# Optimization experiments

Hardware: AMD Instinct MI355X
Metric: run time of the kernel (lower is better)

## Reference

```python
import math
import jax, jax.numpy as jnp
import numpy as np

B, T, C = 4, 2048, 1024
H = 16
D = C // H  # head dim = 64


def setup_inputs() -> dict:
    key = jax.random.key(0)
    ks = jax.random.split(key, 9)
    s = 0.02
    return {
        "x": jax.random.normal(ks[0], (B, T, C), dtype=jnp.float32),
        "Wq": jax.random.normal(ks[1], (C, C), dtype=jnp.float32) * s,
        "bq": jax.random.normal(ks[2], (C,), dtype=jnp.float32) * s,
        "Wk": jax.random.normal(ks[3], (C, C), dtype=jnp.float32) * s,
        "bk": jax.random.normal(ks[4], (C,), dtype=jnp.float32) * s,
        "Wv": jax.random.normal(ks[5], (C, C), dtype=jnp.float32) * s,
        "bv": jax.random.normal(ks[6], (C,), dtype=jnp.float32) * s,
        "Wo": jax.random.normal(ks[7], (C, C), dtype=jnp.float32) * s,
        "bo": jax.random.normal(ks[8], (C,), dtype=jnp.float32) * s,
    }


def reference(x, Wq, bq, Wk, bk, Wv, bv, Wo, bo):
    # Linear projections (torch Linear: x @ W.T + b), split into heads -> [B,H,T,D]
    def heads(y):
        return y.reshape(B, T, H, D).transpose(0, 2, 1, 3)

    q = heads(x @ Wq.T + bq)
    k = heads(x @ Wk.T + bk)
    v = heads(x @ Wv.T + bv)

    # Full [B,H,T,T] score matrix, scaled by 1/sqrt(D) (no mask, dropout=0 / eval)
    scores = jnp.einsum("bhqd,bhkd->bhqk", q, k) / math.sqrt(D)
    attn = jax.nn.softmax(scores, axis=-1)
    out = jnp.einsum("bhqk,bhkd->bhqd", attn, v)
    out = out.transpose(0, 2, 1, 3).reshape(B, T, C)
    return out @ Wo.T + bo
```

## Files before the change

kernel.cpp:

```cpp
#include <hip/hip_runtime.h>
#include <hip/hip_bf16.h>
#include <stdint.h>

#define Bb 4
#define Tt 2048
#define Cc 1024
#define Hh 16
#define Dd 64

using bf16x8 = __bf16 __attribute__((ext_vector_type(8)));
using f32x4  = float  __attribute__((ext_vector_type(4)));
using f32x16 = float  __attribute__((ext_vector_type(16)));
typedef unsigned short u16;
typedef unsigned int   u32;

#if defined(__has_builtin) && __has_builtin(__builtin_amdgcn_exp2f)
#define EXP2F(x) __builtin_amdgcn_exp2f(x)
#else
#define EXP2F(x) exp2f(x)
#endif

#if defined(__has_builtin) && __has_builtin(__builtin_amdgcn_permlane32_swap)
#define PERMLANE32_SWAP(a, b)                                          \
  do {                                                                 \
    auto _r = __builtin_amdgcn_permlane32_swap((a), (b), false, false);\
    (a) = _r[0]; (b) = _r[1];                                          \
  } while (0)
#else
#define PERMLANE32_SWAP(a, b) \
  asm volatile("v_permlane32_swap_b32 %0, %1" : "+v"(a), "+v"(b))
#endif

__device__ __forceinline__ u16 f32_to_bf16(float f) {
  union { float f; unsigned u; } v; v.f = f;
  unsigned r = v.u + 0x7fffu + ((v.u >> 16) & 1u);
  return (u16)(r >> 16);
}

__device__ __forceinline__ void gl2lds16(const u16* g, u16* l) {
  __builtin_amdgcn_global_load_lds(
      (const __attribute__((address_space(1))) u32*)g,
      (__attribute__((address_space(3))) u32*)l, 16, 0, 0);
}

__global__ void cast_f32_to_bf16(const float* __restrict__ in, u16* __restrict__ out, int n) {
  int i = (blockIdx.x * blockDim.x + threadIdx.x) * 4;
  if (i >= n) return;
  float4 v = *reinterpret_cast<const float4*>(in + i);
  ushort4 o;
  o.x = f32_to_bf16(v.x); o.y = f32_to_bf16(v.y);
  o.z = f32_to_bf16(v.z); o.w = f32_to_bf16(v.w);
  *reinterpret_cast<ushort4*>(out + i) = o;
}

__global__ void cast4_f32_to_bf16(const float* __restrict__ w0, const float* __restrict__ w1,
                                  const float* __restrict__ w2, const float* __restrict__ w3,
                                  u16* __restrict__ o0, u16* __restrict__ o1,
                                  u16* __restrict__ o2, u16* __restrict__ o3, int n) {
  const float* in; u16* out;
  switch (blockIdx.y) {
    case 0: in = w0; out = o0; break;
    case 1: in = w1; out = o1; break;
    case 2: in = w2; out = o2; break;
    default: in = w3; out = o3; break;
  }
  int i = (blockIdx.x * blockDim.x + threadIdx.x) * 4;
  if (i >= n) return;
  float4 v = *reinterpret_cast<const float4*>(in + i);
  ushort4 o;
  o.x = f32_to_bf16(v.x); o.y = f32_to_bf16(v.y);
  o.z = f32_to_bf16(v.z); o.w = f32_to_bf16(v.w);
  *reinterpret_cast<ushort4*>(out + i) = o;
}

__global__ __launch_bounds__(256, 2)
void gemm_qkv(const u16* __restrict__ A, const u16* __restrict__ Bqkv,
              const float* __restrict__ bq, const float* __restrict__ bk,
              const float* __restrict__ bv,
              u16* __restrict__ qout, u16* __restrict__ kout, u16* __restrict__ vtout,
              float qscl)
{
  constexpr int K = Cc, BK = 32, LDT = 136;
  __shared__ alignas(16) u16 smem[128 * LDT];
  u16* As = smem;
  u16* Bs = smem + 128 * BK;
  const int tid  = threadIdx.x;
  const int wave = tid >> 6, lane = tid & 63;
  const int row0 = blockIdx.x * 128, col0 = blockIdx.y * 128;
  const int seg  = col0 >> 10;
  const int wm = (wave & 1) * 64, wn = (wave >> 1) * 64;
  const int fr = lane & 15, fk = (lane >> 4) * 8;
  const int srow = lane >> 2, scol = (lane & 3) * 8;

  f32x4 acc[4][4] = {};

  for (int k0 = 0; k0 < K; k0 += BK) {
#pragma unroll
    for (int c = 0; c < 2; ++c) {
      int rg = (wave * 2 + c) * 16;
      gl2lds16(A    + (size_t)(row0 + rg + srow) * K + k0 + scol, &As[rg * BK]);
      gl2lds16(Bqkv + (size_t)(col0 + rg + srow) * K + k0 + scol, &Bs[rg * BK]);
    }
    __syncthreads();
    bf16x8 af[4], bf[4];
#pragma unroll
    for (int i = 0; i < 4; ++i) {
      af[i] = *reinterpret_cast<const bf16x8*>(&As[(wm + i * 16 + fr) * BK + fk]);
      bf[i] = *reinterpret_cast<const bf16x8*>(&Bs[(wn + i * 16 + fr) * BK + fk]);
    }
#pragma unroll
    for (int i = 0; i < 4; ++i)
#pragma unroll
      for (int j = 0; j < 4; ++j)
        acc[i][j] = __builtin_amdgcn_mfma_f32_16x16x32_bf16(af[i], bf[j], acc[i][j], 0, 0, 0);
    __syncthreads();
  }

  const float* bias = (seg == 0) ? bq : ((seg == 1) ? bk : bv);
  const float scale = (seg == 0) ? qscl : 1.0f;
  const int colL0 = col0 & 1023;

  if (seg < 2) {
    u16* outp = (seg == 0) ? qout : kout;
#pragma unroll
    for (int j = 0; j < 4; ++j) {
      int col = colL0 + wn + j * 16 + fr;
      float bvv = bias[col];
#pragma unroll
      for (int i = 0; i < 4; ++i) {
        int rowb = row0 + wm + i * 16 + (lane >> 4) * 4;
#pragma unroll
        for (int r = 0; r < 4; ++r)
          outp[(size_t)(rowb + r) * Cc + col] = f32_to_bf16((acc[i][j][r] + bvv) * scale);
      }
    }
  } else {
#pragma unroll
    for (int j = 0; j < 4; ++j) {
      int lc = wn + j * 16 + fr;
      float bvv = bias[colL0 + lc];
#pragma unroll
      for (int i = 0; i < 4; ++i) {
        int lr = wm + i * 16 + (lane >> 4) * 4;
#pragma unroll
        for (int r = 0; r < 4; ++r)
          smem[lc * LDT + lr + r] = f32_to_bf16(acc[i][j][r] + bvv);
      }
    }
    __syncthreads();
    int lc = tid >> 1, seg2 = tid & 1;
    int col = colL0 + lc;
    int h = col >> 6, d = col & 63;
    int bb = row0 >> 11, t0 = (row0 & 2047) + seg2 * 64;
    u16* dst = vtout + ((size_t)(bb * Hh + h) * Dd + d) * Tt + t0;
    const u16* src = &smem[lc * LDT + seg2 * 64];
#pragma unroll
    for (int g = 0; g < 8; ++g)
      *reinterpret_cast<uint4*>(dst + g * 8) = *reinterpret_cast<const uint4*>(src + g * 8);
  }
}

__global__ __launch_bounds__(256, 2)
void gemm_out(const u16* __restrict__ A, const u16* __restrict__ Bw,
              const float* __restrict__ bias, float* __restrict__ Cout,
              int M, int N, int K)
{
  constexpr int BK = 32;
  __shared__ alignas(16) u16 As[128 * BK];
  __shared__ alignas(16) u16 Bs[128 * BK];
  const int tid  = threadIdx.x;
  const int wave = tid >> 6, lane = tid & 63;
  const int row0 = blockIdx.x * 128, col0 = blockIdx.y * 128;
  const int wm = (wave & 1) * 64, wn = (wave >> 1) * 64;
  const int fr = lane & 15, fk = (lane >> 4) * 8;
  const int srow = lane >> 2, scol = (lane & 3) * 8;

  f32x4 acc[4][4] = {};

  for (int k0 = 0; k0 < K; k0 += BK) {
#pragma unroll
    for (int c = 0; c < 2; ++c) {
      int rg = (wave * 2 + c) * 16;
      gl2lds16(A  + (size_t)(row0 + rg + srow) * K + k0 + scol, &As[rg * BK]);
      gl2lds16(Bw + (size_t)(col0 + rg + srow) * K + k0 + scol, &Bs[rg * BK]);
    }
    __syncthreads();
    bf16x8 af[4], bf[4];
#pragma unroll
    for (int i = 0; i < 4; ++i) {
      af[i] = *reinterpret_cast<const bf16x8*>(&As[(wm + i * 16 + fr) * BK + fk]);
      bf[i] = *reinterpret_cast<const bf16x8*>(&Bs[(wn + i * 16 + fr) * BK + fk]);
    }
#pragma unroll
    for (int i = 0; i < 4; ++i)
#pragma unroll
      for (int j = 0; j < 4; ++j)
        acc[i][j] = __builtin_amdgcn_mfma_f32_16x16x32_bf16(af[i], bf[j], acc[i][j], 0, 0, 0);
    __syncthreads();
  }

#pragma unroll
  for (int j = 0; j < 4; ++j) {
    int col = col0 + wn + j * 16 + fr;
    float bv = bias[col];
#pragma unroll
    for (int i = 0; i < 4; ++i) {
      int rowb = row0 + wm + i * 16 + (lane >> 4) * 4;
#pragma unroll
      for (int r = 0; r < 4; ++r)
        Cout[(size_t)(rowb + r) * N + col] = acc[i][j][r] + bv;
    }
  }
}

__global__ __launch_bounds__(256, 2)
void attn_kernel(const u16* __restrict__ Q, const u16* __restrict__ Kmat,
                 const u16* __restrict__ VT, u16* __restrict__ O) {
  __shared__ alignas(16) unsigned char smem[65536];
  float* OfT = (float*)smem;
  float* Qs  = (float*)(smem + 17408);

  const int tid = threadIdx.x, wave = tid >> 6, lane = tid & 63;
  const int l31 = lane & 31, hi = lane >> 5;
  const int bh = blockIdx.x, qt0 = blockIdx.y;
  const int b = bh >> 4, h = bh & 15;
  const size_t base = (size_t)b * Tt * Cc + (size_t)h * Dd;
  const size_t vtb = (size_t)bh * Dd * Tt;

  bf16x8 qb[2][4];
#pragma unroll
  for (int qt = 0; qt < 2; ++qt) {
    const u16* qp = Q + base + (size_t)(qt0 * 64 + qt * 32 + l31) * Cc + hi * 8;
#pragma unroll
    for (int c = 0; c < 4; ++c)
      qb[qt][c] = *reinterpret_cast<const bf16x8*>(qp + c * 16);
  }

  f32x16 Oacc[2][2] = {};
  float ssum[2] = {0.f, 0.f};

  const u16* pK = Kmat + base + (size_t)(wave * 32 + (lane >> 3)) * Cc +
                  (((lane & 7) ^ (lane >> 3)) << 3);
  const u16* pV[4];
#pragma unroll
  for (int c = 0; c < 4; ++c) {
    int d = wave * 16 + c * 4 + (lane >> 4);
    int cs = (lane & 15) ^ ((c << 2) + (lane >> 4));
    pV[c] = VT + vtb + (size_t)d * Tt + (cs << 3);
  }

  auto STAGE = [&](int buf, int kt) {
    u16* Kd = (u16*)(smem + (buf << 15)) + wave * 2048;
    u16* Vd = Kd + 8192;
    const u16* pk = pK + (size_t)kt * Cc;
#pragma unroll
    for (int c = 0; c < 4; ++c) {
      gl2lds16(pk + (size_t)(c * 8) * Cc, Kd + c * 512);
      gl2lds16(pV[c] + kt, Vd + c * 512);
    }
  };

  STAGE(0, 0);
  __syncthreads();

  int cur = 0;
#pragma unroll 1
  for (int t = 0; t < 16; ++t) {
    if (t < 15) STAGE(cur ^ 1, (t + 1) << 7);

    const u16* Ks = (const u16*)(smem + (cur << 15));
    const u16* Vs = Ks + 8192;

    bf16x8 ka[4], vb[2][2];
    const int key = wave * 32 + l31;
#pragma unroll
    for (int c = 0; c < 4; ++c)
      ka[c] = *reinterpret_cast<const bf16x8*>(
          &Ks[key * 64 + ((((c << 1) + hi) ^ (key & 7)) << 3)]);
#pragma unroll
    for (int k0i = 0; k0i < 2; ++k0i)
#pragma unroll
      for (int dh = 0; dh < 2; ++dh) {
        int drow = dh * 32 + l31;
        int ch = wave * 4 + k0i * 2 + hi;
        vb[k0i][dh] = *reinterpret_cast<const bf16x8*>(
            &Vs[drow * 128 + ((ch ^ (drow & 15)) << 3)]);
      }

#pragma unroll
    for (int qt = 0; qt < 2; ++qt) {
      f32x16 s = {};
#pragma unroll
      for (int c = 0; c < 4; ++c)
        s = __builtin_amdgcn_mfma_f32_32x32x16_bf16(ka[c], qb[qt][c], s, 0, 0, 0);
      unsigned pk8[8];
      float sm = 0.f;
#pragma unroll
      for (int i = 0; i < 8; ++i) {
        float p0 = EXP2F(s[2 * i]), p1 = EXP2F(s[2 * i + 1]);
        sm += p0 + p1;
        union { __hip_bfloat162 h2; unsigned u; } cv;
        cv.h2 = __float22bfloat162_rn(make_float2(p0, p1));
        pk8[i] = cv.u;
      }
      ssum[qt] += sm;
      unsigned a0 = pk8[0], a1 = pk8[1], a2 = pk8[2], a3 = pk8[3];
      unsigned b0 = pk8[4], b1 = pk8[5], b2 = pk8[6], b3 = pk8[7];
      PERMLANE32_SWAP(a0, a2);
      PERMLANE32_SWAP(a1, a3);
      PERMLANE32_SWAP(b0, b2);
      PERMLANE32_SWAP(b1, b3);
      union { unsigned u[4]; bf16x8 v; } plo, phi;
      plo.u[0] = a0; plo.u[1] = a1; plo.u[2] = a2; plo.u[3] = a3;
      phi.u[0] = b0; phi.u[1] = b1; phi.u[2] = b2; phi.u[3] = b3;
      Oacc[qt][0] = __builtin_amdgcn_mfma_f32_32x32x16_bf16(plo.v, vb[0][0], Oacc[qt][0], 0, 0, 0);
      Oacc[qt][1] = __builtin_amdgcn_mfma_f32_32x32x16_bf16(plo.v, vb[0][1], Oacc[qt][1], 0, 0, 0);
      Oacc[qt][0] = __builtin_amdgcn_mfma_f32_32x32x16_bf16(phi.v, vb[1][0], Oacc[qt][0], 0, 0, 0);
      Oacc[qt][1] = __builtin_amdgcn_mfma_f32_32x32x16_bf16(phi.v, vb[1][1], Oacc[qt][1], 0, 0, 0);
    }
    __syncthreads();
    cur ^= 1;
  }

#pragma unroll
  for (int qt = 0; qt < 2; ++qt) {
    float s = ssum[qt];
    s += __shfl_xor(s, 32, 64);
    if (hi == 0) Qs[wave * 64 + qt * 32 + l31] = s;
  }

  for (int w = 0; w < 4; ++w) {
    if (wave == w) {
#pragma unroll
      for (int qt = 0; qt < 2; ++qt)
#pragma unroll
        for (int dh = 0; dh < 2; ++dh) {
          int d = dh * 32 + l31;
          float* rowp = &OfT[d * 68 + qt * 32 + hi * 4];
#pragma unroll
          for (int g = 0; g < 4; ++g) {
            f32x4 v;
            v[0] = Oacc[qt][dh][g * 4 + 0]; v[1] = Oacc[qt][dh][g * 4 + 1];
            v[2] = Oacc[qt][dh][g * 4 + 2]; v[3] = Oacc[qt][dh][g * 4 + 3];
            float* dst = rowp + g * 8;
            if (w == 0) *reinterpret_cast<f32x4*>(dst) = v;
            else {
              f32x4 old = *reinterpret_cast<const f32x4*>(dst);
              *reinterpret_cast<f32x4*>(dst) = old + v;
            }
          }
        }
    }
    __syncthreads();
  }

  {
    int q = tid >> 2, dg = tid & 3;
    float qtot = Qs[q] + Qs[64 + q] + Qs[128 + q] + Qs[192 + q];
    float linv = 1.0f / qtot;
    alignas(16) u16 tmp[16];
#pragma unroll
    for (int i = 0; i < 16; ++i)
      tmp[i] = f32_to_bf16(OfT[(dg * 16 + i) * 68 + q] * linv);
    u16* op = O + base + (size_t)(qt0 * 64 + q) * Cc + dg * 16;
    *reinterpret_cast<uint4*>(op)     = *reinterpret_cast<const uint4*>(tmp);
    *reinterpret_cast<uint4*>(op + 8) = *reinterpret_cast<const uint4*>(tmp + 8);
  }
}

extern "C" void kernel_launch(void* const* d_in, const int* in_sizes, int n_in,
                              void* d_out, int out_size, void* d_ws, size_t ws_size,
                              hipStream_t stream) {
  const float* x  = (const float*)d_in[0];
  const float* Wq = (const float*)d_in[1];
  const float* bq = (const float*)d_in[2];
  const float* Wk = (const float*)d_in[3];
  const float* bk = (const float*)d_in[4];
  const float* Wv = (const float*)d_in[5];
  const float* bv = (const float*)d_in[6];
  const float* Wo = (const float*)d_in[7];
  const float* bo = (const float*)d_in[8];

  const size_t NX = (size_t)Bb * Tt * Cc;
  const size_t NW = (size_t)Cc * Cc;

  u16* ws  = (u16*)d_ws;
  u16* xb  = ws;
  u16* wqb = ws + NX;
  u16* wkb = wqb + NW;
  u16* wvb = wkb + NW;
  u16* wob = wvb + NW;
  u16* qb  = wob + NW;
  u16* kb  = qb + NX;
  u16* vtb = kb + NX;
  u16* attnb = xb;

  cast_f32_to_bf16<<<(int)(NX / 4 / 256), 256, 0, stream>>>(x, xb, (int)NX);
  cast4_f32_to_bf16<<<dim3((unsigned)(NW / 4 / 256), 4), 256, 0, stream>>>(
      Wq, Wk, Wv, Wo, wqb, wkb, wvb, wob, (int)NW);

  const float QSCL = 0.125f * 1.44269504f;
  gemm_qkv<<<dim3(64, 24), 256, 0, stream>>>(xb, wqb, bq, bk, bv, qb, kb, vtb, QSCL);

  attn_kernel<<<dim3(Bb * Hh, Tt / 64), 256, 0, stream>>>(qb, kb, vtb, attnb);

  gemm_out<<<dim3(64, 8), 256, 0, stream>>>(attnb, wob, bo, (float*)d_out,
                                            Bb * Tt, Cc, Cc);
}
```

Before: 307.3 us.

## Split attention waves by query tile and key half, halve LDS for higher occupancy

```diff
diff --git a/kernel.cpp b/kernel.cpp
--- a/kernel.cpp
+++ b/kernel.cpp
@@ -10,6 +10,7 @@
 
 using bf16x8 = __bf16 __attribute__((ext_vector_type(8)));
 using f32x4  = float  __attribute__((ext_vector_type(4)));
+using f32x2  = float  __attribute__((ext_vector_type(2)));
 using f32x16 = float  __attribute__((ext_vector_type(16)));
 typedef unsigned short u16;
 typedef unsigned int   u32;
@@ -213,50 +214,46 @@
   }
 }
 
-__global__ __launch_bounds__(256, 2)
+__global__ __launch_bounds__(256, 4)
 void attn_kernel(const u16* __restrict__ Q, const u16* __restrict__ Kmat,
                  const u16* __restrict__ VT, u16* __restrict__ O) {
-  __shared__ alignas(16) unsigned char smem[65536];
+  __shared__ alignas(16) unsigned char smem[32768];
   float* OfT = (float*)smem;
   float* Qs  = (float*)(smem + 17408);
 
   const int tid = threadIdx.x, wave = tid >> 6, lane = tid & 63;
   const int l31 = lane & 31, hi = lane >> 5;
+  const int qt = wave >> 1, kh = wave & 1;
   const int bh = blockIdx.x, qt0 = blockIdx.y;
   const int b = bh >> 4, h = bh & 15;
   const size_t base = (size_t)b * Tt * Cc + (size_t)h * Dd;
   const size_t vtb = (size_t)bh * Dd * Tt;
 
-  bf16x8 qb[2][4];
-#pragma unroll
-  for (int qt = 0; qt < 2; ++qt) {
+  bf16x8 qb[4];
+  {
     const u16* qp = Q + base + (size_t)(qt0 * 64 + qt * 32 + l31) * Cc + hi * 8;
 #pragma unroll
     for (int c = 0; c < 4; ++c)
-      qb[qt][c] = *reinterpret_cast<const bf16x8*>(qp + c * 16);
-  }
-
-  f32x16 Oacc[2][2] = {};
-  float ssum[2] = {0.f, 0.f};
-
-  const u16* pK = Kmat + base + (size_t)(wave * 32 + (lane >> 3)) * Cc +
+      qb[c] = *reinterpret_cast<const bf16x8*>(qp + c * 16);
+  }
+
+  f32x16 Oacc[2] = {};
+  f32x2 sacc = {0.f, 0.f};
+
+  const u16* pK = Kmat + base + (size_t)(wave * 16 + (lane >> 3)) * Cc +
                   (((lane & 7) ^ (lane >> 3)) << 3);
-  const u16* pV[4];
-#pragma unroll
-  for (int c = 0; c < 4; ++c) {
-    int d = wave * 16 + c * 4 + (lane >> 4);
-    int cs = (lane & 15) ^ ((c << 2) + (lane >> 4));
-    pV[c] = VT + vtb + (size_t)d * Tt + (cs << 3);
-  }
+  const u16* pV = VT + vtb + (size_t)(wave * 16 + (lane >> 3)) * Tt +
+                  (((lane & 7) ^ (lane >> 3)) << 3);
 
   auto STAGE = [&](int buf, int kt) {
-    u16* Kd = (u16*)(smem + (buf << 15)) + wave * 2048;
-    u16* Vd = Kd + 8192;
+    u16* Kd = (u16*)(smem + (buf << 14)) + wave * 1024;
+    u16* Vd = Kd + 4096;
     const u16* pk = pK + (size_t)kt * Cc;
-#pragma unroll
-    for (int c = 0; c < 4; ++c) {
+    const u16* pv = pV + kt;
+#pragma unroll
+    for (int c = 0; c < 2; ++c) {
       gl2lds16(pk + (size_t)(c * 8) * Cc, Kd + c * 512);
-      gl2lds16(pV[c] + kt, Vd + c * 512);
+      gl2lds16(pv + (size_t)(c * 8) * Tt, Vd + c * 512);
     }
   };
 
@@ -265,14 +262,14 @@
 
   int cur = 0;
 #pragma unroll 1
-  for (int t = 0; t < 16; ++t) {
-    if (t < 15) STAGE(cur ^ 1, (t + 1) << 7);
-
-    const u16* Ks = (const u16*)(smem + (cur << 15));
-    const u16* Vs = Ks + 8192;
+  for (int t = 0; t < 32; ++t) {
+    if (t < 31) STAGE(cur ^ 1, (t + 1) << 6);
+
+    const u16* Ks = (const u16*)(smem + (cur << 14));
+    const u16* Vs = Ks + 4096;
 
     bf16x8 ka[4], vb[2][2];
-    const int key = wave * 32 + l31;
+    const int key = kh * 32 + l31;
 #pragma unroll
     for (int c = 0; c < 4; ++c)
       ka[c] = *reinterpret_cast<const bf16x8*>(
@@ -282,81 +279,75 @@
 #pragma unroll
       for (int dh = 0; dh < 2; ++dh) {
         int drow = dh * 32 + l31;
-        int ch = wave * 4 + k0i * 2 + hi;
+        int ch = kh * 4 + k0i * 2 + hi;
         vb[k0i][dh] = *reinterpret_cast<const bf16x8*>(
-            &Vs[drow * 128 + ((ch ^ (drow & 15)) << 3)]);
+            &Vs[drow * 64 + ((ch ^ (drow & 7)) << 3)]);
       }
 
-#pragma unroll
-    for (int qt = 0; qt < 2; ++qt) {
-      f32x16 s = {};
-#pragma unroll
-      for (int c = 0; c < 4; ++c)
-        s = __builtin_amdgcn_mfma_f32_32x32x16_bf16(ka[c], qb[qt][c], s, 0, 0, 0);
-      unsigned pk8[8];
-      float sm = 0.f;
-#pragma unroll
-      for (int i = 0; i < 8; ++i) {
-        float p0 = EXP2F(s[2 * i]), p1 = EXP2F(s[2 * i + 1]);
-        sm += p0 + p1;
-        union { __hip_bfloat162 h2; unsigned u; } cv;
-        cv.h2 = __float22bfloat162_rn(make_float2(p0, p1));
-        pk8[i] = cv.u;
-      }
-      ssum[qt] += sm;
-      unsigned a0 = pk8[0], a1 = pk8[1], a2 = pk8[2], a3 = pk8[3];
-      unsigned b0 = pk8[4], b1 = pk8[5], b2 = pk8[6], b3 = pk8[7];
-      PERMLANE32_SWAP(a0, a2);
-      PERMLANE32_SWAP(a1, a3);
-      PERMLANE32_SWAP(b0, b2);
-      PERMLANE32_SWAP(b1, b3);
-      union { unsigned u[4]; bf16x8 v; } plo, phi;
-      plo.u[0] = a0; plo.u[1] = a1; plo.u[2] = a2; plo.u[3] = a3;
-      phi.u[0] = b0; phi.u[1] = b1; phi.u[2] = b2; phi.u[3] = b3;
-      Oacc[qt][0] = __builtin_amdgcn_mfma_f32_32x32x16_bf16(plo.v, vb[0][0], Oacc[qt][0], 0, 0, 0);
-      Oacc[qt][1] = __builtin_amdgcn_mfma_f32_32x32x16_bf16(plo.v, vb[0][1], Oacc[qt][1], 0, 0, 0);
-      Oacc[qt][0] = __builtin_amdgcn_mfma_f32_32x32x16_bf16(phi.v, vb[1][0], Oacc[qt][0], 0, 0, 0);
-      Oacc[qt][1] = __builtin_amdgcn_mfma_f32_32x32x16_bf16(phi.v, vb[1][1], Oacc[qt][1], 0, 0, 0);
-    }
+    f32x16 s = {};
+#pragma unroll
+    for (int c = 0; c < 4; ++c)
+      s = __builtin_amdgcn_mfma_f32_32x32x16_bf16(ka[c], qb[c], s, 0, 0, 0);
+    unsigned pk8[8];
+#pragma unroll
+    for (int i = 0; i < 8; ++i) {
+      float p0 = EXP2F(s[2 * i]), p1 = EXP2F(s[2 * i + 1]);
+      sacc += (f32x2){p0, p1};
+      union { __hip_bfloat162 h2; unsigned u; } cv;
+      cv.h2 = __float22bfloat162_rn(make_float2(p0, p1));
+      pk8[i] = cv.u;
+    }
+    unsigned a0 = pk8[0], a1 = pk8[1], a2 = pk8[2], a3 = pk8[3];
+    unsigned b0 = pk8[4], b1 = pk8[5], b2 = pk8[6], b3 = pk8[7];
+    PERMLANE32_SWAP(a0, a2);
+    PERMLANE32_SWAP(a1, a3);
+    PERMLANE32_SWAP(b0, b2);
+    PERMLANE32_SWAP(b1, b3);
+    union { unsigned u[4]; bf16x8 v; } plo, phi;
+    plo.u[0] = a0; plo.u[1] = a1; plo.u[2] = a2; plo.u[3] = a3;
+    phi.u[0] = b0; phi.u[1] = b1; phi.u[2] = b2; phi.u[3] = b3;
+    Oacc[0] = __builtin_amdgcn_mfma_f32_32x32x16_bf16(plo.v, vb[0][0], Oacc[0], 0, 0, 0);
+    Oacc[1] = __builtin_amdgcn_mfma_f32_32x32x16_bf16(plo.v, vb[0][1], Oacc[1], 0, 0, 0);
+    Oacc[0] = __builtin_amdgcn_mfma_f32_32x32x16_bf16(phi.v, vb[1][0], Oacc[0], 0, 0, 0);
+    Oacc[1] = __builtin_amdgcn_mfma_f32_32x32x16_bf16(phi.v, vb[1][1], Oacc[1], 0, 0, 0);
+
     __syncthreads();
     cur ^= 1;
   }
 
-#pragma unroll
-  for (int qt = 0; qt < 2; ++qt) {
-    float s = ssum[qt];
+  {
+    float s = sacc[0] + sacc[1];
     s += __shfl_xor(s, 32, 64);
-    if (hi == 0) Qs[wave * 64 + qt * 32 + l31] = s;
-  }
-
-  for (int w = 0; w < 4; ++w) {
-    if (wave == w) {
-#pragma unroll
-      for (int qt = 0; qt < 2; ++qt)
-#pragma unroll
-        for (int dh = 0; dh < 2; ++dh) {
-          int d = dh * 32 + l31;
-          float* rowp = &OfT[d * 68 + qt * 32 + hi * 4];
-#pragma unroll
-          for (int g = 0; g < 4; ++g) {
-            f32x4 v;
-            v[0] = Oacc[qt][dh][g * 4 + 0]; v[1] = Oacc[qt][dh][g * 4 + 1];
-            v[2] = Oacc[qt][dh][g * 4 + 2]; v[3] = Oacc[qt][dh][g * 4 + 3];
-            float* dst = rowp + g * 8;
-            if (w == 0) *reinterpret_cast<f32x4*>(dst) = v;
-            else {
-              f32x4 old = *reinterpret_cast<const f32x4*>(dst);
-              *reinterpret_cast<f32x4*>(dst) = old + v;
-            }
+    if (hi == 0) Qs[wave * 32 + l31] = s;
+  }
+
+#pragma unroll
+  for (int step = 0; step < 2; ++step) {
+    if (kh == step) {
+#pragma unroll
+      for (int dh = 0; dh < 2; ++dh) {
+        int d = dh * 32 + l31;
+        float* rowp = &OfT[d * 68 + qt * 32 + hi * 4];
+#pragma unroll
+        for (int g = 0; g < 4; ++g) {
+          f32x4 v;
+          v[0] = Oacc[dh][g * 4 + 0]; v[1] = Oacc[dh][g * 4 + 1];
+          v[2] = Oacc[dh][g * 4 + 2]; v[3] = Oacc[dh][g * 4 + 3];
+          float* dst = rowp + g * 8;
+          if (step == 0) *reinterpret_cast<f32x4*>(dst) = v;
+          else {
+            f32x4 old = *reinterpret_cast<const f32x4*>(dst);
+            *reinterpret_cast<f32x4*>(dst) = old + v;
           }
         }
+      }
     }
     __syncthreads();
   }
 
   {
     int q = tid >> 2, dg = tid & 3;
-    float qtot = Qs[q] + Qs[64 + q] + Qs[128 + q] + Qs[192 + q];
+    float qtot = Qs[(q >> 5) * 64 + (q & 31)] + Qs[(q >> 5) * 64 + 32 + (q & 31)];
     float linv = 1.0f / qtot;
     alignas(16) u16 tmp[16];
 #pragma unroll
```

Result: faster. 292.3 us (-4.9%).
